# Kernel tuning notes

Hardware: AMD Instinct MI355X
Metric: run time of the kernel (lower is better)

Reference implementation:

```python
import jax, jax.numpy as jnp
import numpy as np

D_MODEL = 1024
H = 16
D_K = D_MODEL // H
D_FF = 4096
EPS = 1e-5
NEG = -1e9


def setup_inputs() -> dict:
    key = jax.random.key(0)
    ks = jax.random.split(key, 12)
    B, S = 4, 1024
    s = 1.0 / np.sqrt(D_MODEL)
    inp = {
        'x': jax.random.normal(ks[0], (B, S, D_MODEL), dtype=jnp.float32),
        'src_mask': jax.random.randint(ks[1], (B, 1, 1, S), 0, 2, dtype=jnp.int32),
        'wq': jax.random.normal(ks[2], (D_MODEL, D_MODEL), dtype=jnp.float32) * s,
        'bq': jnp.zeros((D_MODEL,), jnp.float32),
        'wk': jax.random.normal(ks[3], (D_MODEL, D_MODEL), dtype=jnp.float32) * s,
        'bk': jnp.zeros((D_MODEL,), jnp.float32),
        'wv': jax.random.normal(ks[4], (D_MODEL, D_MODEL), dtype=jnp.float32) * s,
        'bv': jnp.zeros((D_MODEL,), jnp.float32),
        'wo': jax.random.normal(ks[5], (D_MODEL, D_MODEL), dtype=jnp.float32) * s,
        'bo': jnp.zeros((D_MODEL,), jnp.float32),
        'w1': jax.random.normal(ks[6], (D_MODEL, D_FF), dtype=jnp.float32) * s,
        'b1': jnp.zeros((D_FF,), jnp.float32),
        'w2': jax.random.normal(ks[7], (D_FF, D_MODEL), dtype=jnp.float32) * (1.0 / np.sqrt(D_FF)),
        'b2': jnp.zeros((D_MODEL,), jnp.float32),
        'ln1_a': jnp.ones((1,), jnp.float32),
        'ln1_b': jnp.zeros((1,), jnp.float32),
        'ln2_a': jnp.ones((1,), jnp.float32),
        'ln2_b': jnp.zeros((1,), jnp.float32),
    }
    return inp


def _layernorm(x, alpha, bias):
    # Matches torch: mean over last dim; std is UNBIASED (ddof=1); divide by (std + eps).
    mean = jnp.mean(x, axis=-1, keepdims=True)
    std = jnp.sqrt(jnp.var(x, axis=-1, keepdims=True, ddof=1))
    return alpha * (x - mean) / (std + EPS) + bias


def _attention(xn, src_mask, wq, bq, wk, bk, wv, bv, wo, bo):
    B, S, _ = xn.shape
    q = (xn @ wq + bq).reshape(B, S, H, D_K).transpose(0, 2, 1, 3)  # [B,H,S,Dk]
    k = (xn @ wk + bk).reshape(B, S, H, D_K).transpose(0, 2, 1, 3)
    v = (xn @ wv + bv).reshape(B, S, H, D_K).transpose(0, 2, 1, 3)
    scores = jnp.einsum('bhqd,bhkd->bhqk', q, k) / np.sqrt(D_K)
    scores = jnp.where(src_mask == 0, NEG, scores)
    # NOTE: original module applies NO softmax (faithful to source).
    out = jnp.einsum('bhqk,bhkd->bhqd', scores, v)  # [B,H,S,Dk]
    out = out.transpose(0, 2, 1, 3).reshape(B, S, D_MODEL)
    return out @ wo + bo


def reference(x, src_mask, wq, bq, wk, bk, wv, bv, wo, bo,
              w1, b1, w2, b2, ln1_a, ln1_b, ln2_a, ln2_b):
    # Pre-norm residual 1: self-attention
    x = x + _attention(_layernorm(x, ln1_a, ln1_b), src_mask,
                       wq, bq, wk, bk, wv, bv, wo, bo)
    # Pre-norm residual 2: FFN
    xn = _layernorm(x, ln2_a, ln2_b)
    ffn = jax.nn.relu(xn @ w1 + b1) @ w2 + b2
    return x + ffn
```

## Files before the change

kernel.cpp:

```cpp
#include <hip/hip_runtime.h>
#include <hip/hip_bf16.h>
#include <math.h>


#define EPS 1e-5f

typedef __attribute__((ext_vector_type(8))) short bf16x8;
typedef __attribute__((ext_vector_type(4))) float f32x4;
typedef __attribute__((ext_vector_type(8))) int i32x8;
typedef __attribute__((ext_vector_type(4))) int i32x4;

typedef const __attribute__((address_space(1))) unsigned char glob_byte;
typedef __attribute__((address_space(3))) unsigned char lds_byte;

__device__ __forceinline__ void g2l16(const void* g, void* l) {
  __builtin_amdgcn_global_load_lds((glob_byte*)g, (lds_byte*)l, 16, 0, 0);
}

__device__ __forceinline__ unsigned short f2bf(float f) {
  union { float f; unsigned int u; } v; v.f = f;
  return (unsigned short)((v.u + 0x7FFFu + ((v.u >> 16) & 1u)) >> 16);
}
__device__ __forceinline__ float bf2f(unsigned short b) {
  union { unsigned int u; float f; } v; v.u = (unsigned int)b << 16;
  return v.f;
}
__device__ __forceinline__ unsigned int pk_fp8x4(float a, float b, float c, float d) {
  unsigned int p = 0;
  p = __builtin_amdgcn_cvt_pk_fp8_f32(a, b, p, false);
  p = __builtin_amdgcn_cvt_pk_fp8_f32(c, d, p, true);
  return p;
}

__global__ __launch_bounds__(256) void wconv_ln_kernel(
    const float* __restrict__ wq, const float* __restrict__ wk,
    const float* __restrict__ wv, const float* __restrict__ wo,
    const float* __restrict__ w1, const float* __restrict__ w2,
    const float* __restrict__ bq, const float* __restrict__ bk,
    const float* __restrict__ bv, const float* __restrict__ bo,
    unsigned short* __restrict__ wqkvT, unsigned short* __restrict__ woT,
    unsigned char* __restrict__ w1F8, unsigned char* __restrict__ w2F8,
    float* __restrict__ bqkv, float* __restrict__ cboW,
    const float* __restrict__ x, unsigned short* __restrict__ xn,
    const float* __restrict__ ln1a, const float* __restrict__ ln1b) {
  __shared__ float tile[64][65];
  const int bid = blockIdx.x;
  const int t = threadIdx.x;
  if (bid >= 3073) {
    const int row = bid - 3073;
    const float4 v = ((const float4*)(x + (size_t)row * 1024))[t];
    float s  = v.x + v.y + v.z + v.w;
    float ss = v.x * v.x + v.y * v.y + v.z * v.z + v.w * v.w;
#pragma unroll
    for (int off = 32; off > 0; off >>= 1) {
      s  += __shfl_down(s, off, 64);
      ss += __shfl_down(ss, off, 64);
    }
    __shared__ float red[8];
    const int lane = t & 63, wv_ = t >> 6;
    if (lane == 0) { red[wv_] = s; red[4 + wv_] = ss; }
    __syncthreads();
    const float S  = red[0] + red[1] + red[2] + red[3];
    const float SS = red[4] + red[5] + red[6] + red[7];
    const float mean = S * (1.0f / 1024.0f);
    float var = (SS - 1024.0f * mean * mean) * (1.0f / 1023.0f);
    var = fmaxf(var, 0.0f);
    const float scl = ln1a[0] / (sqrtf(var) + EPS);
    const float b = ln1b[0];
    ushort4 o;
    o.x = f2bf((v.x - mean) * scl + b);
    o.y = f2bf((v.y - mean) * scl + b);
    o.z = f2bf((v.z - mean) * scl + b);
    o.w = f2bf((v.w - mean) * scl + b);
    ((ushort4*)(xn + (size_t)row * 1024))[t] = o;
    return;
  }
  if (bid == 3072) {
#pragma unroll
    for (int i = 0; i < 12; ++i) {
      const int n = i * 256 + t;
      bqkv[n] = n < 1024 ? bq[n] : (n < 2048 ? bk[n - 1024] : bv[n - 2048]);
    }
#pragma unroll
    for (int i = 0; i < 16; ++i) {
      const int idx = i * 256 + t;
      cboW[idx] = bo[idx & 1023];
    }
    return;
  }
  const float* src; int K, N, tk, tn;
  unsigned short* dst16 = nullptr; unsigned char* dst8 = nullptr;
  if (bid < 1024) {
    const int m = bid >> 8, loc = bid & 255;
    src = m == 0 ? wq : m == 1 ? wk : m == 2 ? wv : wo;
    dst16 = m == 3 ? woT : (wqkvT + (size_t)m * 1024 * 1024);
    K = 1024; N = 1024; tk = loc >> 4; tn = loc & 15;
  } else if (bid < 2048) {
    const int loc = bid - 1024; src = w1; dst8 = w1F8;
    K = 1024; N = 4096; tk = loc >> 6; tn = loc & 63;
  } else {
    const int loc = bid - 2048; src = w2; dst8 = w2F8;
    K = 4096; N = 1024; tk = loc >> 4; tn = loc & 15;
  }
  const int lr = t >> 4, lc = (t & 15) * 4;
#pragma unroll
  for (int i = 0; i < 4; ++i) {
    const float4 v = *(const float4*)(src + (size_t)(tk * 64 + lr + 16 * i) * N + tn * 64 + lc);
    tile[lr + 16 * i][lc + 0] = v.x;
    tile[lr + 16 * i][lc + 1] = v.y;
    tile[lr + 16 * i][lc + 2] = v.z;
    tile[lr + 16 * i][lc + 3] = v.w;
  }
  __syncthreads();
  const int on = t >> 2, ok = (t & 3) * 16;
#pragma unroll
  for (int jj = 0; jj < 4; ++jj) {
    if (dst8) {
      const unsigned int p = pk_fp8x4(tile[ok + 4 * jj + 0][on], tile[ok + 4 * jj + 1][on],
                                      tile[ok + 4 * jj + 2][on], tile[ok + 4 * jj + 3][on]);
      *(unsigned int*)(dst8 + (size_t)(tn * 64 + on) * K + tk * 64 + ok + 4 * jj) = p;
    } else {
      ushort4 o4;
      o4.x = f2bf(tile[ok + 4 * jj + 0][on]);
      o4.y = f2bf(tile[ok + 4 * jj + 1][on]);
      o4.z = f2bf(tile[ok + 4 * jj + 2][on]);
      o4.w = f2bf(tile[ok + 4 * jj + 3][on]);
      *(ushort4*)(dst16 + (size_t)(tn * 64 + on) * K + tk * 64 + ok + 4 * jj) = o4;
    }
  }
}

template <int TM, int TN, bool OUT_BF16, bool RELU, bool RES, int VSN0,
          bool BATCHB, int RX, int RY>
__global__ __launch_bounds__(256, 4) void mfma_gemm(
    const unsigned short* __restrict__ A, const unsigned short* __restrict__ Bt,
    const float* __restrict__ bias, const float* __restrict__ res,
    void* __restrict__ C0, void* __restrict__ C1,
    int N, int lda, int ldb, int KH) {
  constexpr int WM = 2, WN = 2;
  constexpr int MSPAN = TM / WM, NSPAN = TN / WN;
  constexpr int MI = MSPAN / 16, NJ = NSPAN / 16;
  __shared__ __align__(16) unsigned short As[TM * 64];
  __shared__ __align__(16) unsigned short Bs[TN * 64];
  const int tid = threadIdx.x, lane = tid & 63;
  const int w = tid >> 6;
  const int quad = lane >> 4, col = lane & 15;
  const int wm = w % WM, wn = w / WM;

  int bx = blockIdx.x, by = blockIdx.y;
  {
    const int gx = gridDim.x;
    const int L = bx + gx * by;
    const int r = L & 7, s = L >> 3;
    const int nrx = gx / RX;
    const int rx = r % nrx, ry = r / nrx;
    bx = rx * RX + s % RX;
    by = ry * RY + (s / RX) % RY;
  }
  const int m0 = by * TM, n0 = bx * TN;
  if (BATCHB) {
    const int bb = m0 >> 10;
    Bt += (size_t)bb * 1024 * ldb;
    bias += bb * 1024;
  }

  f32x4 acc[MI][NJ];
  const f32x4 z4 = {0.f, 0.f, 0.f, 0.f};
#pragma unroll
  for (int i = 0; i < MI; ++i)
#pragma unroll
    for (int j = 0; j < NJ; ++j) acc[i][j] = z4;

  for (int k0 = 0; k0 < KH; k0 += 64) {
    __syncthreads();
#pragma unroll
    for (int t = 0; t < TM / 32; ++t) {
      const int s = t * 256 + tid;
      const int r = s >> 3, c = (s & 7) ^ (r & 7);
      g2l16(A + (size_t)(m0 + r) * lda + k0 + c * 8, (void*)(As + s * 8));
    }
#pragma unroll
    for (int t = 0; t < TN / 32; ++t) {
      const int s = t * 256 + tid;
      const int r = s >> 3, c = (s & 7) ^ (r & 7);
      g2l16(Bt + (size_t)(n0 + r) * ldb + k0 + c * 8, (void*)(Bs + s * 8));
    }
    __syncthreads();
#pragma unroll
    for (int h = 0; h < 2; ++h) {
      bf16x8 af[MI], bfr[NJ];
#pragma unroll
      for (int i = 0; i < MI; ++i) {
        const int rr = wm * MSPAN + i * 16 + col;
        af[i] = *(const bf16x8*)(As + rr * 64 + (((h << 2) | quad) ^ (rr & 7)) * 8);
      }
#pragma unroll
      for (int j = 0; j < NJ; ++j) {
        const int rr = wn * NSPAN + j * 16 + col;
        bfr[j] = *(const bf16x8*)(Bs + rr * 64 + (((h << 2) | quad) ^ (rr & 7)) * 8);
      }
#pragma unroll
      for (int i = 0; i < MI; ++i)
#pragma unroll
        for (int j = 0; j < NJ; ++j)
          acc[i][j] = __builtin_amdgcn_mfma_f32_16x16x32_bf16(af[i], bfr[j], acc[i][j], 0, 0, 0);
    }
  }
#pragma unroll
  for (int i = 0; i < MI; ++i) {
    const int mrow = m0 + wm * MSPAN + i * 16 + quad * 4;
#pragma unroll
    for (int j = 0; j < NJ; ++j) {
      const int n = n0 + wn * NSPAN + j * 16 + col;
      const float bn = bias[n];
      if (VSN0 != 0 && n0 >= VSN0) {
        ushort4 o4;
        o4.x = f2bf(acc[i][j][0] + bn);
        o4.y = f2bf(acc[i][j][1] + bn);
        o4.z = f2bf(acc[i][j][2] + bn);
        o4.w = f2bf(acc[i][j][3] + bn);
        *(ushort4*)((unsigned short*)C1 + (size_t)(n - VSN0) * 4096 + mrow) = o4;
        continue;
      }
#pragma unroll
      for (int r = 0; r < 4; ++r) {
        const int m = mrow + r;
        float v = acc[i][j][r] + bn;
        if (RES)  v += res[(size_t)m * N + n];
        if (RELU) v = fmaxf(v, 0.f);
        if (OUT_BF16) ((unsigned short*)C0)[(size_t)m * N + n] = f2bf(v);
        else          ((float*)C0)[(size_t)m * N + n] = v;
      }
    }
  }
}

template <bool FP8OUT, int TN, int RX, int RY>
__global__ __launch_bounds__(256, 4) void mfma_gemm_fp8(
    const unsigned char* __restrict__ A, const unsigned char* __restrict__ Bt,
    const float* __restrict__ bias, const unsigned short* __restrict__ res16,
    void* __restrict__ C0, int N, int lda, int ldb, int KH) {
  constexpr int NSPAN = TN / 2;
  constexpr int NJ = NSPAN / 16;
  __shared__ __align__(16) unsigned char As[128 * 128];
  __shared__ __align__(16) unsigned char Bs[TN * 128];
  const int tid = threadIdx.x, lane = tid & 63;
  const int w = tid >> 6;
  const int quad = lane >> 4, col = lane & 15;
  const int wm = w & 1, wn = w >> 1;

  int bx = blockIdx.x, by = blockIdx.y;
  {
    const int gx = gridDim.x;
    const int L = bx + gx * by;
    const int r = L & 7, s = L >> 3;
    const int nrx = gx / RX;
    const int rx = r % nrx, ry = r / nrx;
    bx = rx * RX + s % RX;
    by = ry * RY + (s / RX) % RY;
  }
  const int m0 = by * 128, n0 = bx * TN;

  f32x4 acc[4][NJ];
  const f32x4 z4 = {0.f, 0.f, 0.f, 0.f};
#pragma unroll
  for (int i = 0; i < 4; ++i)
#pragma unroll
    for (int j = 0; j < NJ; ++j) acc[i][j] = z4;

  for (int k0 = 0; k0 < KH; k0 += 128) {
    __syncthreads();
#pragma unroll
    for (int t = 0; t < 4; ++t) {
      const int s = t * 256 + tid;
      const int r = s >> 3, c = (s & 7) ^ (r & 7);
      g2l16(A + (size_t)(m0 + r) * lda + k0 + c * 16, (void*)(As + s * 16));
    }
#pragma unroll
    for (int t = 0; t < TN / 32; ++t) {
      const int s = t * 256 + tid;
      const int r = s >> 3, c = (s & 7) ^ (r & 7);
      g2l16(Bt + (size_t)(n0 + r) * ldb + k0 + c * 16, (void*)(Bs + s * 16));
    }
    __syncthreads();
    i32x8 af[4];
#pragma unroll
    for (int i = 0; i < 4; ++i) {
      const int rr = wm * 64 + i * 16 + col;
      const i32x4* rowp = (const i32x4*)(As + rr * 128);
      const i32x4 lo = rowp[(2 * quad) ^ (rr & 7)];
      const i32x4 hi = rowp[(2 * quad + 1) ^ (rr & 7)];
      af[i] = __builtin_shufflevector(lo, hi, 0, 1, 2, 3, 4, 5, 6, 7);
    }
#pragma unroll
    for (int j = 0; j < NJ; ++j) {
      const int rr = wn * NSPAN + j * 16 + col;
      const i32x4* rowp = (const i32x4*)(Bs + rr * 128);
      const i32x4 lo = rowp[(2 * quad) ^ (rr & 7)];
      const i32x4 hi = rowp[(2 * quad + 1) ^ (rr & 7)];
      const i32x8 bfj = __builtin_shufflevector(lo, hi, 0, 1, 2, 3, 4, 5, 6, 7);
#pragma unroll
      for (int i = 0; i < 4; ++i)
        acc[i][j] = __builtin_amdgcn_mfma_scale_f32_16x16x128_f8f6f4(
            af[i], bfj, acc[i][j], 0, 0, 0, 0x7F7F7F7Fu, 0, 0x7F7F7F7Fu);
    }
  }
#pragma unroll
  for (int i = 0; i < 4; ++i) {
    const int mrow = m0 + wm * 64 + i * 16 + quad * 4;
#pragma unroll
    for (int j = 0; j < NJ; ++j) {
      const int n = n0 + wn * NSPAN + j * 16 + col;
      const float bn = bias[n];
#pragma unroll
      for (int r = 0; r < 4; ++r) {
        const int m = mrow + r;
        if (FP8OUT) {
          const float v = fmaxf(acc[i][j][r] + bn, 0.f);
          const unsigned int p = __builtin_amdgcn_cvt_pk_fp8_f32(v, v, 0, false);
          ((unsigned char*)C0)[(size_t)m * N + n] = (unsigned char)(p & 0xFF);
        } else {
          const float v = acc[i][j][r] + bn + bf2f(res16[(size_t)m * N + n]);
          ((float*)C0)[(size_t)m * N + n] = v;
        }
      }
    }
  }
}

__global__ __launch_bounds__(256) void ln2_kernel(
    const unsigned short* __restrict__ x1,
    const float* __restrict__ alpha, const float* __restrict__ beta,
    unsigned char* __restrict__ xn2f8) {
  const int row = blockIdx.x, t = threadIdx.x;
  const size_t i = (size_t)row * 256 + t;
  const ushort4 a4 = ((const ushort4*)x1)[i];
  float4 v;
  v.x = bf2f(a4.x); v.y = bf2f(a4.y); v.z = bf2f(a4.z); v.w = bf2f(a4.w);
  float s  = v.x + v.y + v.z + v.w;
  float ss = v.x * v.x + v.y * v.y + v.z * v.z + v.w * v.w;
#pragma unroll
  for (int off = 32; off > 0; off >>= 1) {
    s  += __shfl_down(s, off, 64);
    ss += __shfl_down(ss, off, 64);
  }
  __shared__ float red[8];
  const int lane = t & 63, wv_ = t >> 6;
  if (lane == 0) { red[wv_] = s; red[4 + wv_] = ss; }
  __syncthreads();
  const float S  = red[0] + red[1] + red[2] + red[3];
  const float SS = red[4] + red[5] + red[6] + red[7];
  const float mean = S * (1.0f / 1024.0f);
  float var = (SS - 1024.0f * mean * mean) * (1.0f / 1023.0f);
  var = fmaxf(var, 0.0f);
  const float scl = alpha[0] / (sqrtf(var) + EPS);
  const float bb = beta[0];
  ((unsigned int*)xn2f8)[i] = pk_fp8x4((v.x - mean) * scl + bb,
                                       (v.y - mean) * scl + bb,
                                       (v.z - mean) * scl + bb,
                                       (v.w - mean) * scl + bb);
}

__global__ __launch_bounds__(512) void moment_kernel(
    const unsigned short* __restrict__ kvT, const int* __restrict__ mask,
    const unsigned short* __restrict__ woT,
    unsigned short* __restrict__ Wbt, float* __restrict__ cboW) {
  __shared__ __align__(16) unsigned short Ks[64 * 256];
  __shared__ __align__(16) unsigned short Vs[64 * 256];
  __shared__ __align__(16) unsigned short Ms[64 * 64];
  __shared__ float corrS[64];
  const int tid = threadIdx.x, lane = tid & 63, w = tid >> 6;
  const int quad = lane >> 4, col = lane & 15;
  const int bh = blockIdx.x, b = bh >> 4, h = bh & 15;
  const int w4 = w & 3, ch = w >> 2;
  const int* mrow = mask + b * 1024;
  const f32x4 z4 = {0.f, 0.f, 0.f, 0.f};
  f32x4 acc[2] = {z4, z4};
  float cf[2] = {0.f, 0.f};
  const size_t kbase = (size_t)(h * 64) * 4096 + b * 1024;
  const size_t vbase = (size_t)(1024 + h * 64) * 4096 + b * 1024;

  for (int st = 0; st < 4; ++st) {
    const int t0 = st * 256;
    __syncthreads();
#pragma unroll
    for (int i = 0; i < 4; ++i) {
      const int s = i * 512 + tid;
      const int r = s >> 5, c = (s & 31) ^ (r & 31);
      g2l16(kvT + kbase + (size_t)r * 4096 + t0 + c * 8, (void*)(Ks + s * 8));
      g2l16(kvT + vbase + (size_t)r * 4096 + t0 + c * 8, (void*)(Vs + s * 8));
    }
    __syncthreads();
#pragma unroll
    for (int ss = 0; ss < 4; ++ss) {
#pragma unroll
      for (int kk = 0; kk < 2; ++kk) {
        const int q = ss * 8 + kk * 4 + quad;
        const int gtok = t0 + q * 8;
        const int4 m0 = *(const int4*)(mrow + gtok);
        const int4 m1 = *(const int4*)(mrow + gtok + 4);
        const int rr = w4 * 16 + col;
        bf16x8 af = *(const bf16x8*)(Ks + rr * 256 + ((q ^ (rr & 31)) * 8));
        af[0] = m0.x ? af[0] : (short)0;
        af[1] = m0.y ? af[1] : (short)0;
        af[2] = m0.z ? af[2] : (short)0;
        af[3] = m0.w ? af[3] : (short)0;
        af[4] = m1.x ? af[4] : (short)0;
        af[5] = m1.y ? af[5] : (short)0;
        af[6] = m1.z ? af[6] : (short)0;
        af[7] = m1.w ? af[7] : (short)0;
#pragma unroll
        for (int cl = 0; cl < 2; ++cl) {
          const int vr = (ch * 2 + cl) * 16 + col;
          const bf16x8 vf = *(const bf16x8*)(Vs + vr * 256 + ((q ^ (vr & 31)) * 8));
          if (w4 == 0) {
            if (!m0.x) cf[cl] += bf2f((unsigned short)vf[0]);
            if (!m0.y) cf[cl] += bf2f((unsigned short)vf[1]);
            if (!m0.z) cf[cl] += bf2f((unsigned short)vf[2]);
            if (!m0.w) cf[cl] += bf2f((unsigned short)vf[3]);
            if (!m1.x) cf[cl] += bf2f((unsigned short)vf[4]);
            if (!m1.y) cf[cl] += bf2f((unsigned short)vf[5]);
            if (!m1.z) cf[cl] += bf2f((unsigned short)vf[6]);
            if (!m1.w) cf[cl] += bf2f((unsigned short)vf[7]);
          }
          acc[cl] = __builtin_amdgcn_mfma_f32_16x16x32_bf16(af, vf, acc[cl], 0, 0, 0);
        }
      }
    }
  }
  if (w4 == 0) {
#pragma unroll
    for (int cl = 0; cl < 2; ++cl) {
      float s = cf[cl];
      s += __shfl_xor(s, 16, 64);
      s += __shfl_xor(s, 32, 64);
      if (quad == 0) corrS[(ch * 2 + cl) * 16 + col] = s;
    }
  }
#pragma unroll
  for (int cl = 0; cl < 2; ++cl) {
    const int d2 = (ch * 2 + cl) * 16 + col;
#pragma unroll
    for (int r = 0; r < 4; ++r) {
      const int d1 = w4 * 16 + quad * 4 + r;
      Ms[d1 * 64 + ((d2 >> 3) ^ (d1 & 7)) * 8 + (d2 & 7)] = f2bf(0.125f * acc[cl][r]);
    }
  }
  __syncthreads();

  unsigned short* Wb = Wbt + (size_t)b * 1048576;
#pragma unroll 1
  for (int nt8 = 0; nt8 < 8; ++nt8) {
    const int nbase = (w * 8 + nt8) * 16;
    const bf16x8 af0 = *(const bf16x8*)(woT + (size_t)(nbase + col) * 1024 + h * 64 + quad * 8);
    const bf16x8 af1 = *(const bf16x8*)(woT + (size_t)(nbase + col) * 1024 + h * 64 + 32 + quad * 8);
#pragma unroll
    for (int dt = 0; dt < 4; ++dt) {
      const int d1r = dt * 16 + col;
      const bf16x8 bf0 = *(const bf16x8*)(Ms + d1r * 64 + ((quad ^ (d1r & 7)) * 8));
      const bf16x8 bf1 = *(const bf16x8*)(Ms + d1r * 64 + (((4 + quad) ^ (d1r & 7)) * 8));
      f32x4 a = __builtin_amdgcn_mfma_f32_16x16x32_bf16(af0, bf0, z4, 0, 0, 0);
      a = __builtin_amdgcn_mfma_f32_16x16x32_bf16(af1, bf1, a, 0, 0, 0);
#pragma unroll
      for (int r = 0; r < 4; ++r)
        Wb[(size_t)(nbase + quad * 4 + r) * 1024 + h * 64 + dt * 16 + col] = f2bf(a[r]);
    }
  }
#pragma unroll
  for (int rep = 0; rep < 2; ++rep) {
    const int n = rep * 512 + tid;
    const unsigned short* wrow = woT + (size_t)n * 1024 + h * 64;
    float s = 0.f;
#pragma unroll
    for (int k = 0; k < 64; k += 8) {
      const bf16x8 w8 = *(const bf16x8*)(wrow + k);
      s += bf2f((unsigned short)w8[0]) * corrS[k + 0] +
           bf2f((unsigned short)w8[1]) * corrS[k + 1] +
           bf2f((unsigned short)w8[2]) * corrS[k + 2] +
           bf2f((unsigned short)w8[3]) * corrS[k + 3] +
           bf2f((unsigned short)w8[4]) * corrS[k + 4] +
           bf2f((unsigned short)w8[5]) * corrS[k + 5] +
           bf2f((unsigned short)w8[6]) * corrS[k + 6] +
           bf2f((unsigned short)w8[7]) * corrS[k + 7];
    }
    atomicAdd(cboW + b * 1024 + n, -1e9f * s);
  }
}

extern "C" void kernel_launch(void* const* d_in, const int* in_sizes, int n_in,
                              void* d_out, int out_size, void* d_ws, size_t ws_size,
                              hipStream_t stream) {
  const float* x    = (const float*)d_in[0];
  const int*   mask = (const int*)d_in[1];
  const float* wq = (const float*)d_in[2];
  const float* bq = (const float*)d_in[3];
  const float* wk = (const float*)d_in[4];
  const float* bk = (const float*)d_in[5];
  const float* wv = (const float*)d_in[6];
  const float* bv = (const float*)d_in[7];
  const float* wo = (const float*)d_in[8];
  const float* bo = (const float*)d_in[9];
  const float* w1 = (const float*)d_in[10];
  const float* b1 = (const float*)d_in[11];
  const float* w2 = (const float*)d_in[12];
  const float* b2 = (const float*)d_in[13];
  const float* ln1a = (const float*)d_in[14];
  const float* ln1b = (const float*)d_in[15];
  const float* ln2a = (const float*)d_in[16];
  const float* ln2b = (const float*)d_in[17];
  float* out = (float*)d_out;
  char* W = (char*)d_ws;
  const size_t MB = 1u << 20;

  unsigned short* wqkvT = (unsigned short*)(W + 0 * MB);
  unsigned short* woT   = (unsigned short*)(W + 6 * MB);
  unsigned char*  w1F8  = (unsigned char*)(W + 8 * MB);
  unsigned char*  w2F8  = (unsigned char*)(W + 16 * MB);
  float*          bqkv  = (float*)(W + 24 * MB);
  float*          cboW  = (float*)(W + 24 * MB + 131072);
  unsigned short* xn    = (unsigned short*)(W + 25 * MB);
  unsigned char*  xn2f8 = (unsigned char*)(W + 25 * MB);
  unsigned short* qRM   = (unsigned short*)(W + 33 * MB);
  unsigned short* kvT   = (unsigned short*)(W + 41 * MB);
  unsigned short* Wbt   = (unsigned short*)(W + 57 * MB);
  unsigned short* x1    = (unsigned short*)(W + 65 * MB);
  unsigned char*  hbF8  = (unsigned char*)(W + 41 * MB);

  wconv_ln_kernel<<<7169, 256, 0, stream>>>(wq, wk, wv, wo, w1, w2, bq, bk, bv, bo,
                                            wqkvT, woT, w1F8, w2F8, bqkv, cboW,
                                            x, xn, ln1a, ln1b);
  mfma_gemm<128, 128, true, false, false, 1024, false, 12, 8>
      <<<dim3(24, 32), 256, 0, stream>>>(
      xn, wqkvT, bqkv, nullptr, qRM, kvT, 1024, 1024, 1024, 1024);
  moment_kernel<<<64, 512, 0, stream>>>(kvT, mask, woT, Wbt, cboW);
  mfma_gemm<128, 64, true, false, true, 0, true, 8, 8>
      <<<dim3(16, 32), 256, 0, stream>>>(
      qRM, Wbt, cboW, x, x1, nullptr, 1024, 1024, 1024, 1024);
  ln2_kernel<<<4096, 256, 0, stream>>>(x1, ln2a, ln2b, xn2f8);
  mfma_gemm_fp8<true, 128, 16, 8><<<dim3(32, 32), 256, 0, stream>>>(
      xn2f8, w1F8, b1, nullptr, hbF8, 4096, 1024, 1024, 1024);
  mfma_gemm_fp8<false, 64, 8, 8><<<dim3(16, 32), 256, 0, stream>>>(
      hbF8, w2F8, b2, x1, out, 1024, 4096, 4096, 4096);
}
```

Before: 277.0 us.

## Move attention path GEMMs to FP8 and fold mask correction into LN

Converts the QKV projection, the K^T V moment computation and the Q·Wb GEMM from bf16 to FP8 MFMA (including the scaled 16x16x128 f8f6f4 instruction), shrinking operand traffic and LDS use. The masked-token correction is no longer computed inside the moment kernel: the LN1 pass atomically accumulates the sum of normalized rows of masked tokens plus their count, and the moment kernel multiplies that by a bf16 copy of Wv. K rows for masked tokens are zeroed in the QKV epilogue. This lowers bandwidth and MFMA cost but lowers precision on the attention path, since scores carry no softmax and their values are unbounded. It also adds atomics and an extra memset.

```diff
diff --git a/kernel.cpp b/kernel.cpp
--- a/kernel.cpp
+++ b/kernel.cpp
@@ -30,6 +30,9 @@
   p = __builtin_amdgcn_cvt_pk_fp8_f32(a, b, p, false);
   p = __builtin_amdgcn_cvt_pk_fp8_f32(c, d, p, true);
   return p;
+}
+__device__ __forceinline__ unsigned char f2f8(float v) {
+  return (unsigned char)(__builtin_amdgcn_cvt_pk_fp8_f32(v, v, 0, false) & 0xFF);
 }
 
 __global__ __launch_bounds__(256) void wconv_ln_kernel(
@@ -38,10 +41,13 @@
     const float* __restrict__ w1, const float* __restrict__ w2,
     const float* __restrict__ bq, const float* __restrict__ bk,
     const float* __restrict__ bv, const float* __restrict__ bo,
-    unsigned short* __restrict__ wqkvT, unsigned short* __restrict__ woT,
+    const int* __restrict__ maskG,
+    unsigned char* __restrict__ wqkvF8, unsigned short* __restrict__ woT,
+    unsigned short* __restrict__ wvT16,
     unsigned char* __restrict__ w1F8, unsigned char* __restrict__ w2F8,
     float* __restrict__ bqkv, float* __restrict__ cboW,
-    const float* __restrict__ x, unsigned short* __restrict__ xn,
+    float* __restrict__ smx, float* __restrict__ nmb,
+    const float* __restrict__ x, unsigned char* __restrict__ xnF8,
     const float* __restrict__ ln1a, const float* __restrict__ ln1b) {
   __shared__ float tile[64][65];
   const int bid = blockIdx.x;
@@ -67,12 +73,19 @@
     var = fmaxf(var, 0.0f);
     const float scl = ln1a[0] / (sqrtf(var) + EPS);
     const float b = ln1b[0];
-    ushort4 o;
-    o.x = f2bf((v.x - mean) * scl + b);
-    o.y = f2bf((v.y - mean) * scl + b);
-    o.z = f2bf((v.z - mean) * scl + b);
-    o.w = f2bf((v.w - mean) * scl + b);
-    ((ushort4*)(xn + (size_t)row * 1024))[t] = o;
+    const float o0 = (v.x - mean) * scl + b;
+    const float o1 = (v.y - mean) * scl + b;
+    const float o2 = (v.z - mean) * scl + b;
+    const float o3 = (v.w - mean) * scl + b;
+    ((unsigned int*)xnF8)[(size_t)row * 256 + t] = pk_fp8x4(o0, o1, o2, o3);
+    if (maskG[row] == 0) {
+      float* sp = smx + (row >> 10) * 1024 + t * 4;
+      atomicAdd(sp + 0, o0);
+      atomicAdd(sp + 1, o1);
+      atomicAdd(sp + 2, o2);
+      atomicAdd(sp + 3, o3);
+      if (t == 0) atomicAdd(nmb + (row >> 10), 1.0f);
+    }
     return;
   }
   if (bid == 3072) {
@@ -90,10 +103,12 @@
   }
   const float* src; int K, N, tk, tn;
   unsigned short* dst16 = nullptr; unsigned char* dst8 = nullptr;
+  unsigned short* dstv = nullptr;
   if (bid < 1024) {
     const int m = bid >> 8, loc = bid & 255;
     src = m == 0 ? wq : m == 1 ? wk : m == 2 ? wv : wo;
-    dst16 = m == 3 ? woT : (wqkvT + (size_t)m * 1024 * 1024);
+    if (m == 3) dst16 = woT;
+    else { dst8 = wqkvF8 + (size_t)m * 1024 * 1024; if (m == 2) dstv = wvT16; }
     K = 1024; N = 1024; tk = loc >> 4; tn = loc & 15;
   } else if (bid < 2048) {
     const int loc = bid - 1024; src = w1; dst8 = w1F8;
@@ -119,6 +134,14 @@
       const unsigned int p = pk_fp8x4(tile[ok + 4 * jj + 0][on], tile[ok + 4 * jj + 1][on],
                                       tile[ok + 4 * jj + 2][on], tile[ok + 4 * jj + 3][on]);
       *(unsigned int*)(dst8 + (size_t)(tn * 64 + on) * K + tk * 64 + ok + 4 * jj) = p;
+      if (dstv) {
+        ushort4 o4;
+        o4.x = f2bf(tile[ok + 4 * jj + 0][on]);
+        o4.y = f2bf(tile[ok + 4 * jj + 1][on]);
+        o4.z = f2bf(tile[ok + 4 * jj + 2][on]);
+        o4.w = f2bf(tile[ok + 4 * jj + 3][on]);
+        *(ushort4*)(dstv + (size_t)(tn * 64 + on) * 1024 + tk * 64 + ok + 4 * jj) = o4;
+      }
     } else {
       ushort4 o4;
       o4.x = f2bf(tile[ok + 4 * jj + 0][on]);
@@ -130,22 +153,20 @@
   }
 }
 
-template <int TM, int TN, bool OUT_BF16, bool RELU, bool RES, int VSN0,
-          bool BATCHB, int RX, int RY>
-__global__ __launch_bounds__(256, 4) void mfma_gemm(
-    const unsigned short* __restrict__ A, const unsigned short* __restrict__ Bt,
-    const float* __restrict__ bias, const float* __restrict__ res,
-    void* __restrict__ C0, void* __restrict__ C1,
+template <int EPI, int TN, int RX, int RY>
+__global__ __launch_bounds__(256, 4) void mfma_gemm_fp8(
+    const unsigned char* __restrict__ A, const unsigned char* __restrict__ Bt,
+    const float* __restrict__ bias, const void* __restrict__ resv,
+    void* __restrict__ C0, void* __restrict__ C1, const int* __restrict__ maskG,
     int N, int lda, int ldb, int KH) {
-  constexpr int WM = 2, WN = 2;
-  constexpr int MSPAN = TM / WM, NSPAN = TN / WN;
-  constexpr int MI = MSPAN / 16, NJ = NSPAN / 16;
-  __shared__ __align__(16) unsigned short As[TM * 64];
-  __shared__ __align__(16) unsigned short Bs[TN * 64];
+  constexpr int NSPAN = TN / 2;
+  constexpr int NJ = NSPAN / 16;
+  __shared__ __align__(16) unsigned char As[128 * 128];
+  __shared__ __align__(16) unsigned char Bs[TN * 128];
   const int tid = threadIdx.x, lane = tid & 63;
   const int w = tid >> 6;
   const int quad = lane >> 4, col = lane & 15;
-  const int wm = w % WM, wn = w / WM;
+  const int wm = w & 1, wn = w >> 1;
 
   int bx = blockIdx.x, by = blockIdx.y;
   {
@@ -157,109 +178,12 @@
     bx = rx * RX + s % RX;
     by = ry * RY + (s / RX) % RY;
   }
-  const int m0 = by * TM, n0 = bx * TN;
-  if (BATCHB) {
+  const int m0 = by * 128, n0 = bx * TN;
+  if (EPI == 3) {
     const int bb = m0 >> 10;
     Bt += (size_t)bb * 1024 * ldb;
     bias += bb * 1024;
   }
-
-  f32x4 acc[MI][NJ];
-  const f32x4 z4 = {0.f, 0.f, 0.f, 0.f};
-#pragma unroll
-  for (int i = 0; i < MI; ++i)
-#pragma unroll
-    for (int j = 0; j < NJ; ++j) acc[i][j] = z4;
-
-  for (int k0 = 0; k0 < KH; k0 += 64) {
-    __syncthreads();
-#pragma unroll
-    for (int t = 0; t < TM / 32; ++t) {
-      const int s = t * 256 + tid;
-      const int r = s >> 3, c = (s & 7) ^ (r & 7);
-      g2l16(A + (size_t)(m0 + r) * lda + k0 + c * 8, (void*)(As + s * 8));
-    }
-#pragma unroll
-    for (int t = 0; t < TN / 32; ++t) {
-      const int s = t * 256 + tid;
-      const int r = s >> 3, c = (s & 7) ^ (r & 7);
-      g2l16(Bt + (size_t)(n0 + r) * ldb + k0 + c * 8, (void*)(Bs + s * 8));
-    }
-    __syncthreads();
-#pragma unroll
-    for (int h = 0; h < 2; ++h) {
-      bf16x8 af[MI], bfr[NJ];
-#pragma unroll
-      for (int i = 0; i < MI; ++i) {
-        const int rr = wm * MSPAN + i * 16 + col;
-        af[i] = *(const bf16x8*)(As + rr * 64 + (((h << 2) | quad) ^ (rr & 7)) * 8);
-      }
-#pragma unroll
-      for (int j = 0; j < NJ; ++j) {
-        const int rr = wn * NSPAN + j * 16 + col;
-        bfr[j] = *(const bf16x8*)(Bs + rr * 64 + (((h << 2) | quad) ^ (rr & 7)) * 8);
-      }
-#pragma unroll
-      for (int i = 0; i < MI; ++i)
-#pragma unroll
-        for (int j = 0; j < NJ; ++j)
-          acc[i][j] = __builtin_amdgcn_mfma_f32_16x16x32_bf16(af[i], bfr[j], acc[i][j], 0, 0, 0);
-    }
-  }
-#pragma unroll
-  for (int i = 0; i < MI; ++i) {
-    const int mrow = m0 + wm * MSPAN + i * 16 + quad * 4;
-#pragma unroll
-    for (int j = 0; j < NJ; ++j) {
-      const int n = n0 + wn * NSPAN + j * 16 + col;
-      const float bn = bias[n];
-      if (VSN0 != 0 && n0 >= VSN0) {
-        ushort4 o4;
-        o4.x = f2bf(acc[i][j][0] + bn);
-        o4.y = f2bf(acc[i][j][1] + bn);
-        o4.z = f2bf(acc[i][j][2] + bn);
-        o4.w = f2bf(acc[i][j][3] + bn);
-        *(ushort4*)((unsigned short*)C1 + (size_t)(n - VSN0) * 4096 + mrow) = o4;
-        continue;
-      }
-#pragma unroll
-      for (int r = 0; r < 4; ++r) {
-        const int m = mrow + r;
-        float v = acc[i][j][r] + bn;
-        if (RES)  v += res[(size_t)m * N + n];
-        if (RELU) v = fmaxf(v, 0.f);
-        if (OUT_BF16) ((unsigned short*)C0)[(size_t)m * N + n] = f2bf(v);
-        else          ((float*)C0)[(size_t)m * N + n] = v;
-      }
-    }
-  }
-}
-
-template <bool FP8OUT, int TN, int RX, int RY>
-__global__ __launch_bounds__(256, 4) void mfma_gemm_fp8(
-    const unsigned char* __restrict__ A, const unsigned char* __restrict__ Bt,
-    const float* __restrict__ bias, const unsigned short* __restrict__ res16,
-    void* __restrict__ C0, int N, int lda, int ldb, int KH) {
-  constexpr int NSPAN = TN / 2;
-  constexpr int NJ = NSPAN / 16;
-  __shared__ __align__(16) unsigned char As[128 * 128];
-  __shared__ __align__(16) unsigned char Bs[TN * 128];
-  const int tid = threadIdx.x, lane = tid & 63;
-  const int w = tid >> 6;
-  const int quad = lane >> 4, col = lane & 15;
-  const int wm = w & 1, wn = w >> 1;
-
-  int bx = blockIdx.x, by = blockIdx.y;
-  {
-    const int gx = gridDim.x;
-    const int L = bx + gx * by;
-    const int r = L & 7, s = L >> 3;
-    const int nrx = gx / RX;
-    const int rx = r % nrx, ry = r / nrx;
-    bx = rx * RX + s % RX;
-    by = ry * RY + (s / RX) % RY;
-  }
-  const int m0 = by * 128, n0 = bx * TN;
 
   f32x4 acc[4][NJ];
   const f32x4 z4 = {0.f, 0.f, 0.f, 0.f};
@@ -312,16 +236,39 @@
     for (int j = 0; j < NJ; ++j) {
       const int n = n0 + wn * NSPAN + j * 16 + col;
       const float bn = bias[n];
+      if (EPI == 2) {
+        if (n0 >= 1024) {
+          float v0 = acc[i][j][0] + bn;
+          float v1 = acc[i][j][1] + bn;
+          float v2 = acc[i][j][2] + bn;
+          float v3 = acc[i][j][3] + bn;
+          if (n0 < 2048) {
+            const int4 mq = *(const int4*)(maskG + mrow);
+            v0 = mq.x ? v0 : 0.f;
+            v1 = mq.y ? v1 : 0.f;
+            v2 = mq.z ? v2 : 0.f;
+            v3 = mq.w ? v3 : 0.f;
+          }
+          *(unsigned int*)((unsigned char*)C1 + (size_t)(n - 1024) * 4096 + mrow) =
+              pk_fp8x4(v0, v1, v2, v3);
+        } else {
+#pragma unroll
+          for (int r = 0; r < 4; ++r)
+            ((unsigned char*)C0)[(size_t)(mrow + r) * N + n] = f2f8(acc[i][j][r] + bn);
+        }
+        continue;
+      }
 #pragma unroll
       for (int r = 0; r < 4; ++r) {
         const int m = mrow + r;
-        if (FP8OUT) {
-          const float v = fmaxf(acc[i][j][r] + bn, 0.f);
-          const unsigned int p = __builtin_amdgcn_cvt_pk_fp8_f32(v, v, 0, false);
-          ((unsigned char*)C0)[(size_t)m * N + n] = (unsigned char)(p & 0xFF);
+        if (EPI == 0) {
+          ((unsigned char*)C0)[(size_t)m * N + n] = f2f8(fmaxf(acc[i][j][r] + bn, 0.f));
+        } else if (EPI == 1) {
+          const float v = acc[i][j][r] + bn + bf2f(((const unsigned short*)resv)[(size_t)m * N + n]);
+          ((float*)C0)[(size_t)m * N + n] = v;
         } else {
-          const float v = acc[i][j][r] + bn + bf2f(res16[(size_t)m * N + n]);
-          ((float*)C0)[(size_t)m * N + n] = v;
+          const float v = acc[i][j][r] + bn + ((const float*)resv)[(size_t)m * N + n];
+          ((unsigned short*)C0)[(size_t)m * N + n] = f2bf(v);
         }
       }
     }
@@ -362,79 +309,83 @@
 }
 
 __global__ __launch_bounds__(512) void moment_kernel(
-    const unsigned short* __restrict__ kvT, const int* __restrict__ mask,
-    const unsigned short* __restrict__ woT,
-    unsigned short* __restrict__ Wbt, float* __restrict__ cboW) {
-  __shared__ __align__(16) unsigned short Ks[64 * 256];
-  __shared__ __align__(16) unsigned short Vs[64 * 256];
+    const unsigned char* __restrict__ kvT8, const unsigned short* __restrict__ woT,
+    const unsigned short* __restrict__ wvT16, const float* __restrict__ bqkv,
+    const float* __restrict__ smx, const float* __restrict__ nmb,
+    unsigned char* __restrict__ Wbt8, float* __restrict__ cboW) {
+  __shared__ __align__(16) unsigned char Ks[64 * 512];
+  __shared__ __align__(16) unsigned char Vs[64 * 512];
   __shared__ __align__(16) unsigned short Ms[64 * 64];
+  __shared__ float sS[1024];
   __shared__ float corrS[64];
   const int tid = threadIdx.x, lane = tid & 63, w = tid >> 6;
   const int quad = lane >> 4, col = lane & 15;
   const int bh = blockIdx.x, b = bh >> 4, h = bh & 15;
   const int w4 = w & 3, ch = w >> 2;
-  const int* mrow = mask + b * 1024;
   const f32x4 z4 = {0.f, 0.f, 0.f, 0.f};
+  const size_t kb = (size_t)(h * 64) * 4096 + b * 1024;
+  const size_t vb = (size_t)(1024 + h * 64) * 4096 + b * 1024;
+
+#pragma unroll
+  for (int i = 0; i < 4; ++i) {
+    const int s = i * 512 + tid;
+    const int r = s >> 5, c = (s & 31) ^ (r & 31);
+    g2l16(kvT8 + kb + (size_t)r * 4096 + c * 16, (void*)(Ks + s * 16));
+    g2l16(kvT8 + vb + (size_t)r * 4096 + c * 16, (void*)(Vs + s * 16));
+  }
+  ((float2*)sS)[tid] = ((const float2*)(smx + b * 1024))[tid];
+  __syncthreads();
+
+  {
+    const int d2 = tid >> 3, kq = tid & 7;
+    const unsigned short* wrow = wvT16 + (size_t)(h * 64 + d2) * 1024 + kq * 128;
+    float s = 0.f;
+#pragma unroll
+    for (int jj = 0; jj < 16; ++jj) {
+      const bf16x8 w8 = *(const bf16x8*)(wrow + jj * 8);
+      const float* sp = sS + kq * 128 + jj * 8;
+      s += bf2f((unsigned short)w8[0]) * sp[0] + bf2f((unsigned short)w8[1]) * sp[1] +
+           bf2f((unsigned short)w8[2]) * sp[2] + bf2f((unsigned short)w8[3]) * sp[3] +
+           bf2f((unsigned short)w8[4]) * sp[4] + bf2f((unsigned short)w8[5]) * sp[5] +
+           bf2f((unsigned short)w8[6]) * sp[6] + bf2f((unsigned short)w8[7]) * sp[7];
+    }
+    s += __shfl_xor(s, 1, 64);
+    s += __shfl_xor(s, 2, 64);
+    s += __shfl_xor(s, 4, 64);
+    if ((lane & 7) == 0) corrS[d2] = s + nmb[b] * bqkv[2048 + h * 64 + d2];
+  }
+
   f32x4 acc[2] = {z4, z4};
-  float cf[2] = {0.f, 0.f};
-  const size_t kbase = (size_t)(h * 64) * 4096 + b * 1024;
-  const size_t vbase = (size_t)(1024 + h * 64) * 4096 + b * 1024;
-
-  for (int st = 0; st < 4; ++st) {
-    const int t0 = st * 256;
-    __syncthreads();
-#pragma unroll
-    for (int i = 0; i < 4; ++i) {
-      const int s = i * 512 + tid;
-      const int r = s >> 5, c = (s & 31) ^ (r & 31);
-      g2l16(kvT + kbase + (size_t)r * 4096 + t0 + c * 8, (void*)(Ks + s * 8));
-      g2l16(kvT + vbase + (size_t)r * 4096 + t0 + c * 8, (void*)(Vs + s * 8));
-    }
-    __syncthreads();
-#pragma unroll
-    for (int ss = 0; ss < 4; ++ss) {
-#pragma unroll
-      for (int kk = 0; kk < 2; ++kk) {
-        const int q = ss * 8 + kk * 4 + quad;
-        const int gtok = t0 + q * 8;
-        const int4 m0 = *(const int4*)(mrow + gtok);
-        const int4 m1 = *(const int4*)(mrow + gtok + 4);
-        const int rr = w4 * 16 + col;
-        bf16x8 af = *(const bf16x8*)(Ks + rr * 256 + ((q ^ (rr & 31)) * 8));
-        af[0] = m0.x ? af[0] : (short)0;
-        af[1] = m0.y ? af[1] : (short)0;
-        af[2] = m0.z ? af[2] : (short)0;
-        af[3] = m0.w ? af[3] : (short)0;
-        af[4] = m1.x ? af[4] : (short)0;
-        af[5] = m1.y ? af[5] : (short)0;
-        af[6] = m1.z ? af[6] : (short)0;
-        af[7] = m1.w ? af[7] : (short)0;
-#pragma unroll
-        for (int cl = 0; cl < 2; ++cl) {
-          const int vr = (ch * 2 + cl) * 16 + col;
-          const bf16x8 vf = *(const bf16x8*)(Vs + vr * 256 + ((q ^ (vr & 31)) * 8));
-          if (w4 == 0) {
-            if (!m0.x) cf[cl] += bf2f((unsigned short)vf[0]);
-            if (!m0.y) cf[cl] += bf2f((unsigned short)vf[1]);
-            if (!m0.z) cf[cl] += bf2f((unsigned short)vf[2]);
-            if (!m0.w) cf[cl] += bf2f((unsigned short)vf[3]);
-            if (!m1.x) cf[cl] += bf2f((unsigned short)vf[4]);
-            if (!m1.y) cf[cl] += bf2f((unsigned short)vf[5]);
-            if (!m1.z) cf[cl] += bf2f((unsigned short)vf[6]);
-            if (!m1.w) cf[cl] += bf2f((unsigned short)vf[7]);
-          }
-          acc[cl] = __builtin_amdgcn_mfma_f32_16x16x32_bf16(af, vf, acc[cl], 0, 0, 0);
-        }
+  const int rr = w4 * 16 + col;
+#pragma unroll 1
+  for (int st = 0; st < 2; ++st) {
+    if (st) {
+      __syncthreads();
+#pragma unroll
+      for (int i = 0; i < 4; ++i) {
+        const int s = i * 512 + tid;
+        const int r = s >> 5, c = (s & 31) ^ (r & 31);
+        g2l16(kvT8 + kb + (size_t)r * 4096 + 512 + c * 16, (void*)(Ks + s * 16));
+        g2l16(kvT8 + vb + (size_t)r * 4096 + 512 + c * 16, (void*)(Vs + s * 16));
       }
-    }
-  }
-  if (w4 == 0) {
-#pragma unroll
-    for (int cl = 0; cl < 2; ++cl) {
-      float s = cf[cl];
-      s += __shfl_xor(s, 16, 64);
-      s += __shfl_xor(s, 32, 64);
-      if (quad == 0) corrS[(ch * 2 + cl) * 16 + col] = s;
+      __syncthreads();
+    }
+#pragma unroll
+    for (int q = 0; q < 4; ++q) {
+      const i32x4* rowpK = (const i32x4*)(Ks + rr * 512);
+      const i32x4 klo = rowpK[(q * 8 + 2 * quad) ^ (rr & 31)];
+      const i32x4 khi = rowpK[(q * 8 + 2 * quad + 1) ^ (rr & 31)];
+      const i32x8 af = __builtin_shufflevector(klo, khi, 0, 1, 2, 3, 4, 5, 6, 7);
+#pragma unroll
+      for (int cl = 0; cl < 2; ++cl) {
+        const int vr = (ch * 2 + cl) * 16 + col;
+        const i32x4* rowpV = (const i32x4*)(Vs + vr * 512);
+        const i32x4 vlo = rowpV[(q * 8 + 2 * quad) ^ (vr & 31)];
+        const i32x4 vhi = rowpV[(q * 8 + 2 * quad + 1) ^ (vr & 31)];
+        const i32x8 vf = __builtin_shufflevector(vlo, vhi, 0, 1, 2, 3, 4, 5, 6, 7);
+        acc[cl] = __builtin_amdgcn_mfma_scale_f32_16x16x128_f8f6f4(
+            af, vf, acc[cl], 0, 0, 0, 0x7F7F7F7Fu, 0, 0x7F7F7F7Fu);
+      }
     }
   }
 #pragma unroll
@@ -448,7 +399,7 @@
   }
   __syncthreads();
 
-  unsigned short* Wb = Wbt + (size_t)b * 1048576;
+  unsigned char* Wb8 = Wbt8 + (size_t)b * 1048576;
 #pragma unroll 1
   for (int nt8 = 0; nt8 < 8; ++nt8) {
     const int nbase = (w * 8 + nt8) * 16;
@@ -463,7 +414,7 @@
       a = __builtin_amdgcn_mfma_f32_16x16x32_bf16(af1, bf1, a, 0, 0, 0);
 #pragma unroll
       for (int r = 0; r < 4; ++r)
-        Wb[(size_t)(nbase + quad * 4 + r) * 1024 + h * 64 + dt * 16 + col] = f2bf(a[r]);
+        Wb8[(size_t)(nbase + quad * 4 + r) * 1024 + h * 64 + dt * 16 + col] = f2f8(a[r]);
     }
   }
 #pragma unroll
@@ -512,33 +463,35 @@
   char* W = (char*)d_ws;
   const size_t MB = 1u << 20;
 
-  unsigned short* wqkvT = (unsigned short*)(W + 0 * MB);
-  unsigned short* woT   = (unsigned short*)(W + 6 * MB);
-  unsigned char*  w1F8  = (unsigned char*)(W + 8 * MB);
-  unsigned char*  w2F8  = (unsigned char*)(W + 16 * MB);
-  float*          bqkv  = (float*)(W + 24 * MB);
-  float*          cboW  = (float*)(W + 24 * MB + 131072);
-  unsigned short* xn    = (unsigned short*)(W + 25 * MB);
-  unsigned char*  xn2f8 = (unsigned char*)(W + 25 * MB);
-  unsigned short* qRM   = (unsigned short*)(W + 33 * MB);
-  unsigned short* kvT   = (unsigned short*)(W + 41 * MB);
-  unsigned short* Wbt   = (unsigned short*)(W + 57 * MB);
-  unsigned short* x1    = (unsigned short*)(W + 65 * MB);
-  unsigned char*  hbF8  = (unsigned char*)(W + 41 * MB);
-
+  unsigned char*  wqkvF8 = (unsigned char*)(W + 0 * MB);
+  unsigned short* woT    = (unsigned short*)(W + 3 * MB);
+  unsigned short* wvT16  = (unsigned short*)(W + 5 * MB);
+  unsigned char*  w1F8   = (unsigned char*)(W + 7 * MB);
+  unsigned char*  w2F8   = (unsigned char*)(W + 11 * MB);
+  float*          bqkv   = (float*)(W + 15 * MB);
+  float*          cboW   = (float*)(W + 15 * MB + 65536);
+  float*          smx    = (float*)(W + 15 * MB + 131072);
+  float*          nmb    = (float*)(W + 15 * MB + 147456);
+  unsigned char*  xnF8   = (unsigned char*)(W + 16 * MB);
+  unsigned char*  Q8     = (unsigned char*)(W + 20 * MB);
+  unsigned char*  kvT8   = (unsigned char*)(W + 24 * MB);
+  unsigned char*  Wbt8   = (unsigned char*)(W + 32 * MB);
+  unsigned short* x1     = (unsigned short*)(W + 36 * MB);
+  unsigned char*  xn2f8  = (unsigned char*)(W + 44 * MB);
+  unsigned char*  hbF8   = (unsigned char*)(W + 48 * MB);
+
+  hipMemsetAsync(W + 15 * MB + 131072, 0, 16384 + 16, stream);
   wconv_ln_kernel<<<7169, 256, 0, stream>>>(wq, wk, wv, wo, w1, w2, bq, bk, bv, bo,
-                                            wqkvT, woT, w1F8, w2F8, bqkv, cboW,
-                                            x, xn, ln1a, ln1b);
-  mfma_gemm<128, 128, true, false, false, 1024, false, 12, 8>
-      <<<dim3(24, 32), 256, 0, stream>>>(
-      xn, wqkvT, bqkv, nullptr, qRM, kvT, 1024, 1024, 1024, 1024);
-  moment_kernel<<<64, 512, 0, stream>>>(kvT, mask, woT, Wbt, cboW);
-  mfma_gemm<128, 64, true, false, true, 0, true, 8, 8>
-      <<<dim3(16, 32), 256, 0, stream>>>(
-      qRM, Wbt, cboW, x, x1, nullptr, 1024, 1024, 1024, 1024);
+                                            mask, wqkvF8, woT, wvT16, w1F8, w2F8,
+                                            bqkv, cboW, smx, nmb, x, xnF8, ln1a, ln1b);
+  mfma_gemm_fp8<2, 128, 12, 8><<<dim3(24, 32), 256, 0, stream>>>(
+      xnF8, wqkvF8, bqkv, nullptr, Q8, kvT8, mask, 1024, 1024, 1024, 1024);
+  moment_kernel<<<64, 512, 0, stream>>>(kvT8, woT, wvT16, bqkv, smx, nmb, Wbt8, cboW);
+  mfma_gemm_fp8<3, 64, 8, 8><<<dim3(16, 32), 256, 0, stream>>>(
+      Q8, Wbt8, cboW, x, x1, nullptr, nullptr, 1024, 1024, 1024, 1024);
   ln2_kernel<<<4096, 256, 0, stream>>>(x1, ln2a, ln2b, xn2f8);
-  mfma_gemm_fp8<true, 128, 16, 8><<<dim3(32, 32), 256, 0, stream>>>(
-      xn2f8, w1F8, b1, nullptr, hbF8, 4096, 1024, 1024, 1024);
-  mfma_gemm_fp8<false, 64, 8, 8><<<dim3(16, 32), 256, 0, stream>>>(
-      hbF8, w2F8, b2, x1, out, 1024, 4096, 4096, 4096);
-}
+  mfma_gemm_fp8<0, 128, 16, 8><<<dim3(32, 32), 256, 0, stream>>>(
+      xn2f8, w1F8, b1, nullptr, hbF8, nullptr, nullptr, 4096, 1024, 1024, 1024);
+  mfma_gemm_fp8<1, 64, 8, 8><<<dim3(16, 32), 256, 0, stream>>>(
+      hbF8, w2F8, b2, x1, out, nullptr, nullptr, 1024, 4096, 4096, 4096);
+}
```

Result: slower. 344.9 us (+24.5%).
